# Optimization experiments

Measured on AMD Instinct MI355X. Metric: run time of the kernel, lower is better.

The kernel has to match this reference:

```python
import jax, jax.numpy as jnp
import numpy as np

N_NODES = 100000
N_EDGES = 3200000
IN_SIZE = 256
HID_SIZE = 256
OUT_SIZE = 64


def setup_inputs() -> dict:
    key = jax.random.key(0)
    ks = jax.random.split(key, 8)
    X = jax.random.normal(ks[0], (N_NODES, IN_SIZE), dtype=jnp.float32)
    edge_vals = jax.random.uniform(ks[1], (N_EDGES,), dtype=jnp.float32)
    # xavier-uniform-ish init for weights
    lim1 = float(np.sqrt(6.0 / (IN_SIZE + HID_SIZE)))
    W1 = jax.random.uniform(ks[2], (IN_SIZE, HID_SIZE), minval=-lim1, maxval=lim1, dtype=jnp.float32)
    b1 = jnp.zeros((HID_SIZE,), dtype=jnp.float32)
    lim2 = float(np.sqrt(6.0 / (HID_SIZE + OUT_SIZE)))
    W2 = jax.random.uniform(ks[3], (HID_SIZE, OUT_SIZE), minval=-lim2, maxval=lim2, dtype=jnp.float32)
    b2 = jnp.zeros((OUT_SIZE,), dtype=jnp.float32)
    row = jnp.sort(jax.random.randint(ks[4], (N_EDGES,), 0, N_NODES, dtype=jnp.int32))
    col = jax.random.randint(ks[5], (N_EDGES,), 0, N_NODES, dtype=jnp.int32)
    return {"X": X, "edge_vals": edge_vals, "W1": W1, "b1": b1,
            "W2": W2, "b2": b2, "row": row, "col": col}


def reference(X, edge_vals, W1, b1, W2, b2, row, col):
    """2-layer GCN (eval mode, dropout = identity).

    A is a sparse NxN matrix in COO form: A[row[e], col[e]] = edge_vals[e].
    Layer: relu(A @ (X @ W1) + b1); output: A @ (h @ W2) + b2.
    """
    n = X.shape[0]

    def spmm(dense):  # (A @ dense): gather columns, scale, segment-sum over rows
        gathered = edge_vals[:, None] * dense[col]        # [E, F]
        return jax.ops.segment_sum(gathered, row, num_segments=n)

    h = spmm(X @ W1) + b1          # [N, HID]
    h = jax.nn.relu(h)
    out = spmm(h @ W2) + b2        # [N, OUT]
    return out
```

## Files before the change

### kernel.cpp

```cpp
#include <hip/hip_runtime.h>


constexpr int IN_SIZE = 256;
constexpr int HID = 256;
constexpr int OUTF = 64;

typedef __bf16 bf16x8 __attribute__((ext_vector_type(8)));
typedef float f32x4 __attribute__((ext_vector_type(4)));

__device__ __forceinline__ ushort f2b(float f) {
    uint u = __float_as_uint(f);
    uint r = (u + 0x7fffu + ((u >> 16) & 1u)) >> 16;
    return (ushort)r;
}

__device__ __forceinline__ void fma4(float* a, uint word, float w) {
    a[0] += w * (float)(word & 0xffu);
    a[1] += w * (float)((word >> 8) & 0xffu);
    a[2] += w * (float)((word >> 16) & 0xffu);
    a[3] += w * (float)(word >> 24);
}

__global__ void setup_kernel(const int* __restrict__ row, int* __restrict__ rp,
                             const float* __restrict__ W1, ushort* __restrict__ W1T,
                             const float* __restrict__ W2, ushort* __restrict__ W2T,
                             int n, int E, int rpB) {
    int b = blockIdx.x;
    if (b < rpB) {
        int i = b * 256 + threadIdx.x;
        if (i > n) return;
        int lo = 0, hi = E;
        while (lo < hi) {
            int mid = (lo + hi) >> 1;
            if (row[mid] < i) lo = mid + 1; else hi = mid;
        }
        rp[i] = lo;
    } else if (b < rpB + 256) {
        int nn = b - rpB;
        int k = threadIdx.x;
        W1T[(size_t)nn * 256 + k] = f2b(W1[(size_t)k * 256 + nn]);
    } else {
        int nn = b - rpB - 256;
        int k = threadIdx.x;
        W2T[(size_t)nn * 256 + k] = f2b(W2[(size_t)k * 64 + nn]);
    }
}

__global__ void prep_edges(const float* __restrict__ vals, const int* __restrict__ col,
                           const float* __restrict__ s, int2* __restrict__ ew,
                           int E, int shift) {
    int e = blockIdx.x * 256 + threadIdx.x;
    if (e >= E) return;
    int c = col[e];
    ew[e] = make_int2(c << shift, __float_as_int(vals[e] * s[c]));
}

__global__ __launch_bounds__(512)
void gemm1_q(const float* __restrict__ A, const ushort* __restrict__ Bt,
             unsigned char* __restrict__ Q, float* __restrict__ s1, int M) {
    constexpr int K = 256;
    __shared__ ushort As[128 * 40];
    __shared__ ushort Bs[256 * 40];
    __shared__ float red[4][128];
    __shared__ float fin[128];
    const int tid = threadIdx.x;
    const int wave = tid >> 6, lane = tid & 63;
    const int quad = lane >> 4, l = lane & 15;
    const int wr = wave >> 2, wc = wave & 3;
    const int m0 = blockIdx.x * 128;

    const int ar = tid >> 2;
    const int ak = (tid & 3) * 8;
    const size_t aoff = (size_t)min(m0 + ar, M - 1) * K + ak;
    const int bn = tid >> 2;
    const int bkp = (tid & 3) * 8;
    const size_t boff0 = (size_t)bn * K + bkp;
    const size_t boff1 = (size_t)(bn + 128) * K + bkp;

    f32x4 acc[4][4] = {};

    float4 a0 = *(const float4*)(A + aoff);
    float4 a1 = *(const float4*)(A + aoff + 4);
    uint4 bv0 = *(const uint4*)(Bt + boff0);
    uint4 bv1 = *(const uint4*)(Bt + boff1);

    for (int k0 = 0; k0 < K; k0 += 32) {
        uint4 pa;
        pa.x = (uint)f2b(a0.x) | ((uint)f2b(a0.y) << 16);
        pa.y = (uint)f2b(a0.z) | ((uint)f2b(a0.w) << 16);
        pa.z = (uint)f2b(a1.x) | ((uint)f2b(a1.y) << 16);
        pa.w = (uint)f2b(a1.z) | ((uint)f2b(a1.w) << 16);
        __syncthreads();
        *(uint4*)&As[ar * 40 + ak] = pa;
        *(uint4*)&Bs[bn * 40 + bkp] = bv0;
        *(uint4*)&Bs[(bn + 128) * 40 + bkp] = bv1;
        __syncthreads();

        if (k0 + 32 < K) {
            a0 = *(const float4*)(A + aoff + k0 + 32);
            a1 = *(const float4*)(A + aoff + k0 + 36);
            bv0 = *(const uint4*)(Bt + boff0 + k0 + 32);
            bv1 = *(const uint4*)(Bt + boff1 + k0 + 32);
        }

        bf16x8 af[4], bfr[4];
#pragma unroll
        for (int mt = 0; mt < 4; ++mt)
            af[mt] = *(const bf16x8*)&As[(wr * 64 + mt * 16 + l) * 40 + quad * 8];
#pragma unroll
        for (int nt = 0; nt < 4; ++nt)
            bfr[nt] = *(const bf16x8*)&Bs[(wc * 64 + nt * 16 + l) * 40 + quad * 8];
#pragma unroll
        for (int mt = 0; mt < 4; ++mt)
#pragma unroll
            for (int nt = 0; nt < 4; ++nt)
                acc[mt][nt] = __builtin_amdgcn_mfma_f32_16x16x32_bf16(
                    af[mt], bfr[nt], acc[mt][nt], 0, 0, 0);
    }

    float rmax[4][4];
#pragma unroll
    for (int mt = 0; mt < 4; ++mt)
#pragma unroll
        for (int reg = 0; reg < 4; ++reg) {
            float m = 0.f;
#pragma unroll
            for (int nt = 0; nt < 4; ++nt)
                m = fmaxf(m, fabsf(acc[mt][nt][reg]));
            rmax[mt][reg] = m;
        }
#pragma unroll
    for (int s = 1; s <= 8; s <<= 1)
#pragma unroll
        for (int mt = 0; mt < 4; ++mt)
#pragma unroll
            for (int reg = 0; reg < 4; ++reg)
                rmax[mt][reg] = fmaxf(rmax[mt][reg], __shfl_xor(rmax[mt][reg], s));
    if (l < 4) {
#pragma unroll
        for (int mt = 0; mt < 4; ++mt)
            red[wc][wr * 64 + mt * 16 + quad * 4 + l] = rmax[mt][l];
    }
    __syncthreads();
    if (tid < 128) {
        float m = fmaxf(fmaxf(red[0][tid], red[1][tid]),
                        fmaxf(red[2][tid], red[3][tid]));
        fin[tid] = m;
        int r = m0 + tid;
        if (r < M) s1[r] = m * (1.f / 127.f);
    }
    __syncthreads();

#pragma unroll
    for (int mt = 0; mt < 4; ++mt)
#pragma unroll
        for (int reg = 0; reg < 4; ++reg) {
            int rl = wr * 64 + mt * 16 + quad * 4 + reg;
            int r = m0 + rl;
            if (r >= M) continue;
            float m = fin[rl];
            float inv = m > 0.f ? 127.f / m : 0.f;
#pragma unroll
            for (int nt = 0; nt < 4; ++nt) {
                int c = wc * 64 + nt * 16 + l;
                Q[(size_t)r * 256 + c] =
                    (unsigned char)((int)rintf(acc[mt][nt][reg] * inv) + 128);
            }
        }
}

__global__ __launch_bounds__(256, 4)
void gemm2_q(const ushort* __restrict__ A, const ushort* __restrict__ Bt,
             unsigned char* __restrict__ Q, float* __restrict__ s2, int M) {
    constexpr int K = 256;
    __shared__ ushort As[128 * 40];
    __shared__ ushort Bs[64 * 40];
    __shared__ float red[2][128];
    __shared__ float fin[128];
    const int tid = threadIdx.x;
    const int wave = tid >> 6, lane = tid & 63;
    const int quad = lane >> 4, l = lane & 15;
    const int wr = wave >> 1, wc = wave & 1;
    const int m0 = blockIdx.x * 128;

    const int crow = tid >> 2;
    const int cpart = (tid & 3) * 8;
    const size_t aoff0 = (size_t)min(m0 + crow, M - 1) * K + cpart;
    const size_t aoff1 = (size_t)min(m0 + crow + 64, M - 1) * K + cpart;
    const size_t boff  = (size_t)crow * K + cpart;

    f32x4 acc[4][2] = {};

    uint4 a0 = *(const uint4*)(A + aoff0);
    uint4 a1 = *(const uint4*)(A + aoff1);
    uint4 b0 = *(const uint4*)(Bt + boff);

    for (int k0 = 0; k0 < K; k0 += 32) {
        __syncthreads();
        *(uint4*)&As[crow * 40 + cpart] = a0;
        *(uint4*)&As[(crow + 64) * 40 + cpart] = a1;
        *(uint4*)&Bs[crow * 40 + cpart] = b0;
        __syncthreads();

        if (k0 + 32 < K) {
            a0 = *(const uint4*)(A + aoff0 + k0 + 32);
            a1 = *(const uint4*)(A + aoff1 + k0 + 32);
            b0 = *(const uint4*)(Bt + boff + k0 + 32);
        }

        bf16x8 af[4], bfr[2];
        const ushort* ab = &As[(wr * 64 + l) * 40 + quad * 8];
#pragma unroll
        for (int mt = 0; mt < 4; ++mt)
            af[mt] = *(const bf16x8*)(ab + mt * 16 * 40);
        const ushort* bb = &Bs[(wc * 32 + l) * 40 + quad * 8];
#pragma unroll
        for (int nt = 0; nt < 2; ++nt)
            bfr[nt] = *(const bf16x8*)(bb + nt * 16 * 40);
#pragma unroll
        for (int mt = 0; mt < 4; ++mt)
#pragma unroll
            for (int nt = 0; nt < 2; ++nt)
                acc[mt][nt] = __builtin_amdgcn_mfma_f32_16x16x32_bf16(
                    af[mt], bfr[nt], acc[mt][nt], 0, 0, 0);
    }

    float rmax[4][4];
#pragma unroll
    for (int mt = 0; mt < 4; ++mt)
#pragma unroll
        for (int reg = 0; reg < 4; ++reg)
            rmax[mt][reg] = fmaxf(fabsf(acc[mt][0][reg]), fabsf(acc[mt][1][reg]));
#pragma unroll
    for (int s = 1; s <= 8; s <<= 1)
#pragma unroll
        for (int mt = 0; mt < 4; ++mt)
#pragma unroll
            for (int reg = 0; reg < 4; ++reg)
                rmax[mt][reg] = fmaxf(rmax[mt][reg], __shfl_xor(rmax[mt][reg], s));
    if (l < 4) {
#pragma unroll
        for (int mt = 0; mt < 4; ++mt)
            red[wc][wr * 64 + mt * 16 + quad * 4 + l] = rmax[mt][l];
    }
    __syncthreads();
    if (tid < 128) {
        float m = fmaxf(red[0][tid], red[1][tid]);
        fin[tid] = m;
        int r = m0 + tid;
        if (r < M) s2[r] = m * (1.f / 127.f);
    }
    __syncthreads();

#pragma unroll
    for (int mt = 0; mt < 4; ++mt)
#pragma unroll
        for (int reg = 0; reg < 4; ++reg) {
            int rl = wr * 64 + mt * 16 + quad * 4 + reg;
            int r = m0 + rl;
            if (r >= M) continue;
            float m = fin[rl];
            float inv = m > 0.f ? 127.f / m : 0.f;
#pragma unroll
            for (int nt = 0; nt < 2; ++nt) {
                int c = wc * 32 + nt * 16 + l;
                Q[(size_t)r * 64 + c] =
                    (unsigned char)((int)rintf(acc[mt][nt][reg] * inv) + 128);
            }
        }
}

__global__ __launch_bounds__(256)
void spmm1_q(const unsigned char* __restrict__ Q, const int2* __restrict__ ew,
             const int* __restrict__ rp, const float* __restrict__ bias,
             ushort* __restrict__ H, int n) {
    const int wave = threadIdx.x >> 6;
    const int lane = threadIdx.x & 63;
    const int node = blockIdx.x * 4 + wave;
    if (node >= n) return;
    const int e0 = rp[node], e1 = rp[node + 1];
    const int g = lane >> 4;
    const int fb = (lane & 15) * 16;

    float acc[16] = {};
    float sumw = 0.f;
    int e = e0;
    for (; e + 16 <= e1; e += 16) {
#pragma unroll
        for (int u = 0; u < 4; ++u) {
            int2 m = ew[e + u * 4 + g];
            float w = __int_as_float(m.y);
            uint4 qv = *(const uint4*)(Q + (size_t)(uint)m.x + fb);
            sumw += w;
            fma4(&acc[0], qv.x, w);
            fma4(&acc[4], qv.y, w);
            fma4(&acc[8], qv.z, w);
            fma4(&acc[12], qv.w, w);
        }
    }
    for (; e < e1; e += 4) {
        int idx = e + g;
        int2 m = ew[idx];
        bool ok = idx < e1;
        uint off = ok ? (uint)m.x : 0u;
        float w = ok ? __int_as_float(m.y) : 0.f;
        uint4 qv = *(const uint4*)(Q + (size_t)off + fb);
        sumw += w;
        fma4(&acc[0], qv.x, w);
        fma4(&acc[4], qv.y, w);
        fma4(&acc[8], qv.z, w);
        fma4(&acc[12], qv.w, w);
    }

#pragma unroll
    for (int s = 16; s <= 32; s <<= 1) {
#pragma unroll
        for (int j = 0; j < 16; ++j)
            acc[j] += __shfl_xor(acc[j], s);
        sumw += __shfl_xor(sumw, s);
    }

    if (g == 0) {
        const int f0 = (lane & 15) * 16;
        float4 b0 = *(const float4*)(bias + f0);
        float4 b1 = *(const float4*)(bias + f0 + 4);
        float4 b2 = *(const float4*)(bias + f0 + 8);
        float4 b3 = *(const float4*)(bias + f0 + 12);
        float bb[16] = {b0.x, b0.y, b0.z, b0.w, b1.x, b1.y, b1.z, b1.w,
                        b2.x, b2.y, b2.z, b2.w, b3.x, b3.y, b3.z, b3.w};
        float fix = -128.f * sumw;
        ushort r[16];
#pragma unroll
        for (int j = 0; j < 16; ++j)
            r[j] = f2b(fmaxf(acc[j] + fix + bb[j], 0.f));
        uint4 w0, w1;
        w0.x = (uint)r[0] | ((uint)r[1] << 16);
        w0.y = (uint)r[2] | ((uint)r[3] << 16);
        w0.z = (uint)r[4] | ((uint)r[5] << 16);
        w0.w = (uint)r[6] | ((uint)r[7] << 16);
        w1.x = (uint)r[8] | ((uint)r[9] << 16);
        w1.y = (uint)r[10] | ((uint)r[11] << 16);
        w1.z = (uint)r[12] | ((uint)r[13] << 16);
        w1.w = (uint)r[14] | ((uint)r[15] << 16);
        *(uint4*)(H + (size_t)node * 256 + f0) = w0;
        *(uint4*)(H + (size_t)node * 256 + f0 + 8) = w1;
    }
}

__global__ __launch_bounds__(256)
void spmm2_q(const unsigned char* __restrict__ Q, const int2* __restrict__ ew,
             const int* __restrict__ rp, const float* __restrict__ bias,
             float* __restrict__ O, int n) {
    const int wave = threadIdx.x >> 6;
    const int lane = threadIdx.x & 63;
    const int node = blockIdx.x * 4 + wave;
    if (node >= n) return;
    const int e0 = rp[node], e1 = rp[node + 1];
    const int g = lane >> 3;
    const int fb = (lane & 7) * 8;

    float acc[8] = {};
    float sumw = 0.f;
    int e = e0;
    for (; e + 16 <= e1; e += 16) {
#pragma unroll
        for (int u = 0; u < 2; ++u) {
            int2 m = ew[e + u * 8 + g];
            float w = __int_as_float(m.y);
            uint2 qv = *(const uint2*)(Q + (size_t)(uint)m.x + fb);
            sumw += w;
            fma4(&acc[0], qv.x, w);
            fma4(&acc[4], qv.y, w);
        }
    }
    for (; e < e1; e += 8) {
        int idx = e + g;
        int2 m = ew[idx];
        bool ok = idx < e1;
        uint off = ok ? (uint)m.x : 0u;
        float w = ok ? __int_as_float(m.y) : 0.f;
        uint2 qv = *(const uint2*)(Q + (size_t)off + fb);
        sumw += w;
        fma4(&acc[0], qv.x, w);
        fma4(&acc[4], qv.y, w);
    }

#pragma unroll
    for (int s = 8; s <= 32; s <<= 1) {
#pragma unroll
        for (int j = 0; j < 8; ++j)
            acc[j] += __shfl_xor(acc[j], s);
        sumw += __shfl_xor(sumw, s);
    }

    if (g == 0) {
        const int f0 = (lane & 7) * 8;
        float4 b0 = *(const float4*)(bias + f0);
        float4 b1 = *(const float4*)(bias + f0 + 4);
        float fix = -128.f * sumw;
        float4 o0, o1;
        o0.x = acc[0] + fix + b0.x;
        o0.y = acc[1] + fix + b0.y;
        o0.z = acc[2] + fix + b0.z;
        o0.w = acc[3] + fix + b0.w;
        o1.x = acc[4] + fix + b1.x;
        o1.y = acc[5] + fix + b1.y;
        o1.z = acc[6] + fix + b1.z;
        o1.w = acc[7] + fix + b1.w;
        *(float4*)(O + (size_t)node * 64 + f0) = o0;
        *(float4*)(O + (size_t)node * 64 + f0 + 4) = o1;
    }
}

static inline size_t alignup(size_t x) { return (x + 255) & ~(size_t)255; }

extern "C" void kernel_launch(void* const* d_in, const int* in_sizes, int n_in,
                              void* d_out, int out_size, void* d_ws, size_t ws_size,
                              hipStream_t stream) {
    const float* X  = (const float*)d_in[0];
    const float* ev = (const float*)d_in[1];
    const float* W1 = (const float*)d_in[2];
    const float* b1 = (const float*)d_in[3];
    const float* W2 = (const float*)d_in[4];
    const float* b2 = (const float*)d_in[5];
    const int*  row = (const int*)d_in[6];
    const int*  col = (const int*)d_in[7];
    float* out = (float*)d_out;

    const int n = in_sizes[0] / IN_SIZE;
    const int E = in_sizes[1];

    char* p = (char*)d_ws;
    ushort* H    = (ushort*)p; p += alignup((size_t)n * HID * 2);
    unsigned char* Q1 = (unsigned char*)p; p += alignup((size_t)n * HID);
    float*  s1   = (float*)p;  p += alignup((size_t)n * 4);
    unsigned char* Q2 = (unsigned char*)p; p += alignup((size_t)n * OUTF);
    float*  s2   = (float*)p;  p += alignup((size_t)n * 4);
    ushort* W1T  = (ushort*)p; p += alignup((size_t)IN_SIZE * HID * 2);
    ushort* W2T  = (ushort*)p; p += alignup((size_t)HID * OUTF * 2);
    int*    rp   = (int*)p;    p += alignup((size_t)(n + 1) * 4);
    int2*   ewb  = (int2*)p;   p += alignup((size_t)(E + 16) * 8);

    const int rpB = (n + 1 + 255) / 256;
    setup_kernel<<<rpB + 256 + 64, 256, 0, stream>>>(row, rp, W1, W1T, W2, W2T,
                                                     n, E, rpB);

    gemm1_q<<<(n + 127) / 128, 512, 0, stream>>>(X, W1T, Q1, s1, n);

    prep_edges<<<(E + 255) / 256, 256, 0, stream>>>(ev, col, s1, ewb, E, 8);

    spmm1_q<<<(n + 3) / 4, 256, 0, stream>>>(Q1, ewb, rp, b1, H, n);

    gemm2_q<<<(n + 127) / 128, 256, 0, stream>>>(H, W2T, Q2, s2, n);

    prep_edges<<<(E + 255) / 256, 256, 0, stream>>>(ev, col, s2, ewb, E, 6);

    spmm2_q<<<(n + 3) / 4, 256, 0, stream>>>(Q2, ewb, rp, b2, out, n);
}
```

Baseline: 454.8 us.

## Keep full weight matrix in swizzled LDS and stream A directly into registers

Both dense GEMM kernels now load the whole transposed weight matrix into LDS once, using an XOR swizzle. Each wave loads its A fragments straight from global memory into registers, so A is no longer staged through shared memory and the per-k-step barriers go away. In gemm2 each wave now owns full 64-column rows, so the row max for quantisation is computed within the wave and the cross-wave LDS reduction is dropped. The trade-off is a large LDS footprint in gemm1 (128KB), which limits occupancy, plus uncoalesced per-lane A loads.

```diff
diff --git a/kernel.cpp b/kernel.cpp
--- a/kernel.cpp
+++ b/kernel.cpp
@@ -19,6 +19,15 @@
     a[1] += w * (float)((word >> 8) & 0xffu);
     a[2] += w * (float)((word >> 16) & 0xffu);
     a[3] += w * (float)(word >> 24);
+}
+
+__device__ __forceinline__ bf16x8 pack8(float4 a, float4 b) {
+    union { uint4 u; bf16x8 h; } cv;
+    cv.u.x = (uint)f2b(a.x) | ((uint)f2b(a.y) << 16);
+    cv.u.y = (uint)f2b(a.z) | ((uint)f2b(a.w) << 16);
+    cv.u.z = (uint)f2b(b.x) | ((uint)f2b(b.y) << 16);
+    cv.u.w = (uint)f2b(b.z) | ((uint)f2b(b.w) << 16);
+    return cv.h;
 }
 
 __global__ void setup_kernel(const int* __restrict__ row, int* __restrict__ rp,
@@ -58,58 +67,54 @@
 __global__ __launch_bounds__(512)
 void gemm1_q(const float* __restrict__ A, const ushort* __restrict__ Bt,
              unsigned char* __restrict__ Q, float* __restrict__ s1, int M) {
-    constexpr int K = 256;
-    __shared__ ushort As[128 * 40];
-    __shared__ ushort Bs[256 * 40];
-    __shared__ float red[4][128];
-    __shared__ float fin[128];
+    __shared__ uint4 Wlds[8192];
     const int tid = threadIdx.x;
     const int wave = tid >> 6, lane = tid & 63;
     const int quad = lane >> 4, l = lane & 15;
     const int wr = wave >> 2, wc = wave & 3;
     const int m0 = blockIdx.x * 128;
 
-    const int ar = tid >> 2;
-    const int ak = (tid & 3) * 8;
-    const size_t aoff = (size_t)min(m0 + ar, M - 1) * K + ak;
-    const int bn = tid >> 2;
-    const int bkp = (tid & 3) * 8;
-    const size_t boff0 = (size_t)bn * K + bkp;
-    const size_t boff1 = (size_t)(bn + 128) * K + bkp;
+    for (int i = tid; i < 8192; i += 512) {
+        uint4 v = ((const uint4*)Bt)[i];
+        Wlds[(i & ~31) | ((i & 31) ^ ((i >> 5) & 7))] = v;
+    }
+    __syncthreads();
+
+    size_t abase[4];
+#pragma unroll
+    for (int mt = 0; mt < 4; ++mt) {
+        int r = min(m0 + wr * 64 + mt * 16 + l, M - 1);
+        abase[mt] = (size_t)r * 256 + quad * 8;
+    }
 
     f32x4 acc[4][4] = {};
-
-    float4 a0 = *(const float4*)(A + aoff);
-    float4 a1 = *(const float4*)(A + aoff + 4);
-    uint4 bv0 = *(const uint4*)(Bt + boff0);
-    uint4 bv1 = *(const uint4*)(Bt + boff1);
-
-    for (int k0 = 0; k0 < K; k0 += 32) {
-        uint4 pa;
-        pa.x = (uint)f2b(a0.x) | ((uint)f2b(a0.y) << 16);
-        pa.y = (uint)f2b(a0.z) | ((uint)f2b(a0.w) << 16);
-        pa.z = (uint)f2b(a1.x) | ((uint)f2b(a1.y) << 16);
-        pa.w = (uint)f2b(a1.z) | ((uint)f2b(a1.w) << 16);
-        __syncthreads();
-        *(uint4*)&As[ar * 40 + ak] = pa;
-        *(uint4*)&Bs[bn * 40 + bkp] = bv0;
-        *(uint4*)&Bs[(bn + 128) * 40 + bkp] = bv1;
-        __syncthreads();
-
-        if (k0 + 32 < K) {
-            a0 = *(const float4*)(A + aoff + k0 + 32);
-            a1 = *(const float4*)(A + aoff + k0 + 36);
-            bv0 = *(const uint4*)(Bt + boff0 + k0 + 32);
-            bv1 = *(const uint4*)(Bt + boff1 + k0 + 32);
-        }
-
-        bf16x8 af[4], bfr[4];
+    float4 ra[4], rb[4];
+#pragma unroll
+    for (int mt = 0; mt < 4; ++mt) {
+        ra[mt] = *(const float4*)(A + abase[mt]);
+        rb[mt] = *(const float4*)(A + abase[mt] + 4);
+    }
+
+#pragma unroll
+    for (int kstep = 0; kstep < 8; ++kstep) {
+        bf16x8 af[4];
 #pragma unroll
         for (int mt = 0; mt < 4; ++mt)
-            af[mt] = *(const bf16x8*)&As[(wr * 64 + mt * 16 + l) * 40 + quad * 8];
-#pragma unroll
-        for (int nt = 0; nt < 4; ++nt)
-            bfr[nt] = *(const bf16x8*)&Bs[(wc * 64 + nt * 16 + l) * 40 + quad * 8];
+            af[mt] = pack8(ra[mt], rb[mt]);
+        if (kstep < 7) {
+#pragma unroll
+            for (int mt = 0; mt < 4; ++mt) {
+                ra[mt] = *(const float4*)(A + abase[mt] + (kstep + 1) * 32);
+                rb[mt] = *(const float4*)(A + abase[mt] + (kstep + 1) * 32 + 4);
+            }
+        }
+        bf16x8 bfr[4];
+#pragma unroll
+        for (int nt = 0; nt < 4; ++nt) {
+            int c = wc * 64 + nt * 16 + l;
+            int idx = c * 32 + (((kstep << 2) + quad) ^ (c & 7));
+            bfr[nt] = *(const bf16x8*)&Wlds[idx];
+        }
 #pragma unroll
         for (int mt = 0; mt < 4; ++mt)
 #pragma unroll
@@ -118,6 +123,10 @@
                     af[mt], bfr[nt], acc[mt][nt], 0, 0, 0);
     }
 
+    __syncthreads();
+    float* red = (float*)Wlds;
+    float* fin = red + 512;
+
     float rmax[4][4];
 #pragma unroll
     for (int mt = 0; mt < 4; ++mt)
@@ -139,12 +148,12 @@
     if (l < 4) {
 #pragma unroll
         for (int mt = 0; mt < 4; ++mt)
-            red[wc][wr * 64 + mt * 16 + quad * 4 + l] = rmax[mt][l];
+            red[wc * 128 + wr * 64 + mt * 16 + quad * 4 + l] = rmax[mt][l];
     }
     __syncthreads();
     if (tid < 128) {
-        float m = fmaxf(fmaxf(red[0][tid], red[1][tid]),
-                        fmaxf(red[2][tid], red[3][tid]));
+        float m = fmaxf(fmaxf(red[tid], red[128 + tid]),
+                        fmaxf(red[256 + tid], red[384 + tid]));
         fin[tid] = m;
         int r = m0 + tid;
         if (r < M) s1[r] = m * (1.f / 127.f);
@@ -172,98 +181,87 @@
 __global__ __launch_bounds__(256, 4)
 void gemm2_q(const ushort* __restrict__ A, const ushort* __restrict__ Bt,
              unsigned char* __restrict__ Q, float* __restrict__ s2, int M) {
-    constexpr int K = 256;
-    __shared__ ushort As[128 * 40];
-    __shared__ ushort Bs[64 * 40];
-    __shared__ float red[2][128];
-    __shared__ float fin[128];
+    __shared__ uint4 Wlds[2048];
     const int tid = threadIdx.x;
     const int wave = tid >> 6, lane = tid & 63;
     const int quad = lane >> 4, l = lane & 15;
-    const int wr = wave >> 1, wc = wave & 1;
-    const int m0 = blockIdx.x * 128;
-
-    const int crow = tid >> 2;
-    const int cpart = (tid & 3) * 8;
-    const size_t aoff0 = (size_t)min(m0 + crow, M - 1) * K + cpart;
-    const size_t aoff1 = (size_t)min(m0 + crow + 64, M - 1) * K + cpart;
-    const size_t boff  = (size_t)crow * K + cpart;
-
-    f32x4 acc[4][2] = {};
-
-    uint4 a0 = *(const uint4*)(A + aoff0);
-    uint4 a1 = *(const uint4*)(A + aoff1);
-    uint4 b0 = *(const uint4*)(Bt + boff);
-
-    for (int k0 = 0; k0 < K; k0 += 32) {
-        __syncthreads();
-        *(uint4*)&As[crow * 40 + cpart] = a0;
-        *(uint4*)&As[(crow + 64) * 40 + cpart] = a1;
-        *(uint4*)&Bs[crow * 40 + cpart] = b0;
-        __syncthreads();
-
-        if (k0 + 32 < K) {
-            a0 = *(const uint4*)(A + aoff0 + k0 + 32);
-            a1 = *(const uint4*)(A + aoff1 + k0 + 32);
-            b0 = *(const uint4*)(Bt + boff + k0 + 32);
-        }
-
-        bf16x8 af[4], bfr[2];
-        const ushort* ab = &As[(wr * 64 + l) * 40 + quad * 8];
-#pragma unroll
-        for (int mt = 0; mt < 4; ++mt)
-            af[mt] = *(const bf16x8*)(ab + mt * 16 * 40);
-        const ushort* bb = &Bs[(wc * 32 + l) * 40 + quad * 8];
-#pragma unroll
-        for (int nt = 0; nt < 2; ++nt)
-            bfr[nt] = *(const bf16x8*)(bb + nt * 16 * 40);
-#pragma unroll
-        for (int mt = 0; mt < 4; ++mt)
-#pragma unroll
-            for (int nt = 0; nt < 2; ++nt)
+    const int r0 = blockIdx.x * 128 + wave * 32;
+
+    for (int i = tid; i < 2048; i += 256) {
+        uint4 v = ((const uint4*)Bt)[i];
+        Wlds[(i & ~31) | ((i & 31) ^ ((i >> 5) & 7))] = v;
+    }
+    __syncthreads();
+
+    size_t abase[2];
+#pragma unroll
+    for (int mt = 0; mt < 2; ++mt) {
+        int r = min(r0 + mt * 16 + l, M - 1);
+        abase[mt] = (size_t)r * 256 + quad * 8;
+    }
+
+    f32x4 acc[2][4] = {};
+    uint4 ra[2];
+#pragma unroll
+    for (int mt = 0; mt < 2; ++mt)
+        ra[mt] = *(const uint4*)(A + abase[mt]);
+
+#pragma unroll
+    for (int kstep = 0; kstep < 8; ++kstep) {
+        bf16x8 af[2];
+#pragma unroll
+        for (int mt = 0; mt < 2; ++mt)
+            af[mt] = *(const bf16x8*)&ra[mt];
+        if (kstep < 7) {
+#pragma unroll
+            for (int mt = 0; mt < 2; ++mt)
+                ra[mt] = *(const uint4*)(A + abase[mt] + (kstep + 1) * 32);
+        }
+        bf16x8 bfr[4];
+#pragma unroll
+        for (int nt = 0; nt < 4; ++nt) {
+            int c = nt * 16 + l;
+            int idx = c * 32 + (((kstep << 2) + quad) ^ (c & 7));
+            bfr[nt] = *(const bf16x8*)&Wlds[idx];
+        }
+#pragma unroll
+        for (int mt = 0; mt < 2; ++mt)
+#pragma unroll
+            for (int nt = 0; nt < 4; ++nt)
                 acc[mt][nt] = __builtin_amdgcn_mfma_f32_16x16x32_bf16(
                     af[mt], bfr[nt], acc[mt][nt], 0, 0, 0);
     }
 
-    float rmax[4][4];
-#pragma unroll
-    for (int mt = 0; mt < 4; ++mt)
-#pragma unroll
-        for (int reg = 0; reg < 4; ++reg)
-            rmax[mt][reg] = fmaxf(fabsf(acc[mt][0][reg]), fabsf(acc[mt][1][reg]));
+    float rmax[2][4];
+#pragma unroll
+    for (int mt = 0; mt < 2; ++mt)
+#pragma unroll
+        for (int reg = 0; reg < 4; ++reg) {
+            float m = fmaxf(fabsf(acc[mt][0][reg]), fabsf(acc[mt][1][reg]));
+            m = fmaxf(m, fabsf(acc[mt][2][reg]));
+            m = fmaxf(m, fabsf(acc[mt][3][reg]));
+            rmax[mt][reg] = m;
+        }
 #pragma unroll
     for (int s = 1; s <= 8; s <<= 1)
 #pragma unroll
-        for (int mt = 0; mt < 4; ++mt)
+        for (int mt = 0; mt < 2; ++mt)
 #pragma unroll
             for (int reg = 0; reg < 4; ++reg)
                 rmax[mt][reg] = fmaxf(rmax[mt][reg], __shfl_xor(rmax[mt][reg], s));
-    if (l < 4) {
-#pragma unroll
-        for (int mt = 0; mt < 4; ++mt)
-            red[wc][wr * 64 + mt * 16 + quad * 4 + l] = rmax[mt][l];
-    }
-    __syncthreads();
-    if (tid < 128) {
-        float m = fmaxf(red[0][tid], red[1][tid]);
-        fin[tid] = m;
-        int r = m0 + tid;
-        if (r < M) s2[r] = m * (1.f / 127.f);
-    }
-    __syncthreads();
-
-#pragma unroll
-    for (int mt = 0; mt < 4; ++mt)
+
+#pragma unroll
+    for (int mt = 0; mt < 2; ++mt)
 #pragma unroll
         for (int reg = 0; reg < 4; ++reg) {
-            int rl = wr * 64 + mt * 16 + quad * 4 + reg;
-            int r = m0 + rl;
+            int r = r0 + mt * 16 + quad * 4 + reg;
             if (r >= M) continue;
-            float m = fin[rl];
+            float m = rmax[mt][reg];
+            if (l == 0) s2[r] = m * (1.f / 127.f);
             float inv = m > 0.f ? 127.f / m : 0.f;
 #pragma unroll
-            for (int nt = 0; nt < 2; ++nt) {
-                int c = wc * 32 + nt * 16 + l;
+            for (int nt = 0; nt < 4; ++nt) {
+                int c = nt * 16 + l;
                 Q[(size_t)r * 64 + c] =
                     (unsigned char)((int)rintf(acc[mt][nt][reg] * inv) + 128);
             }
```

New measurement: 484.5 us. 1.07x slower.
